# Kernel optimization log

Measured on AMD Instinct MI355X. Metric: run time of the kernel, lower is better.

## Reference

```python
import jax, jax.numpy as jnp
import numpy as np
from jax import lax

LAMBDA_SPATIAL = 0.5
SIGMA = 100.0
B, N, D = 16, 2048, 768


def setup_inputs() -> dict:
    key = jax.random.key(0)
    k1, k2 = jax.random.split(key)
    features = jax.random.normal(k1, (B, N, D), dtype=jnp.float32)
    coords = jax.random.uniform(k2, (B, N, 2), dtype=jnp.float32)
    return {"features": features, "coords": coords}


def _compute_similarity(features, coords):
    # features: [B,N,D], coords: [B,N,2] -> similarity [B,N,N]
    fn = features / jnp.maximum(jnp.linalg.norm(features, axis=-1, keepdims=True), 1e-12)
    semantic = jnp.einsum('bnd,bmd->bnm', fn, fn)
    diff = coords[:, :, None, :] - coords[:, None, :, :]   # [B,N,N,2]
    sq_dist = jnp.sum(diff * diff, axis=-1)                # d_ij^2
    spatial = jnp.exp(-sq_dist / (SIGMA ** 2))
    return semantic + LAMBDA_SPATIAL * spatial


def _greedy_order(sim):
    # sim: [N,N] -> order [N] int32 greedy nearest-neighbor traversal
    n = sim.shape[0]
    start = jnp.argmax(jnp.sum(sim, axis=1)).astype(jnp.int32)
    visited0 = jnp.zeros((n,), dtype=bool).at[start].set(True)

    def step(carry, _):
        cur, visited = carry
        row = jnp.where(visited, -jnp.inf, jnp.take(sim, cur, axis=0))
        nxt = jnp.argmax(row).astype(jnp.int32)
        return (nxt, visited.at[nxt].set(True)), nxt

    _, rest = lax.scan(step, (start, visited0), None, length=n - 1)
    return jnp.concatenate([start[None], rest])


def reference(features, coords):
    similarity = _compute_similarity(features, coords)          # [B,N,N]
    order = jax.vmap(_greedy_order)(similarity)                 # [B,N]
    reordered = jnp.take_along_axis(features, order[:, :, None], axis=1)  # [B,N,D]
    return reordered, order
```

## Files before the change

### kernel.cpp

```cpp
#include <hip/hip_runtime.h>
#include <math.h>

#define BATCH 16
#define NPTS  2048
#define DIM   768
#define NCH   24

typedef unsigned long long ull;
typedef float f32x4 __attribute__((ext_vector_type(4)));
typedef short bf8 __attribute__((ext_vector_type(8)));

__device__ __forceinline__ unsigned bfr(float x) {
  unsigned u = __float_as_uint(x);
  return (u + 0x7FFFu + ((u >> 16) & 1u)) & 0xFFFF0000u;
}
__device__ __forceinline__ unsigned short f2bf(float x) {
  unsigned u = __float_as_uint(x);
  u += 0x7FFFu + ((u >> 16) & 1u);
  return (unsigned short)(u >> 16);
}

__global__ void normalize_k(const float* __restrict__ feat, float* __restrict__ fn, int cs) {
  const int rn = blockIdx.x;
  const int ci = rn >> 11, n = rn & (NPTS - 1);
  const float* src = feat + ((size_t)(cs + ci) * NPTS + n) * DIM;
  const int t = threadIdx.x;
  float f0 = src[t], f1 = src[t + 256], f2 = src[t + 512];
  double s = (double)f0 * (double)f0 + (double)f1 * (double)f1 + (double)f2 * (double)f2;
  for (int off = 32; off > 0; off >>= 1) s += __shfl_down(s, off);
  __shared__ double ps[4];
  __shared__ double rbc;
  const int lane = t & 63, wid = t >> 6;
  if (lane == 0) ps[wid] = s;
  __syncthreads();
  if (t == 0) {
    double tot = ps[0] + ps[1] + ps[2] + ps[3];
    rbc = fmax(sqrt(tot), 1e-12);
  }
  __syncthreads();
  const double r = rbc;
  float* dst = fn + ((size_t)ci * NPTS + n) * DIM;
  dst[t]       = (float)((double)f0 / r);
  dst[t + 256] = (float)((double)f1 / r);
  dst[t + 512] = (float)((double)f2 / r);
}

__global__ __launch_bounds__(256, 1) void gemm_k(const float* __restrict__ fn,
                                                 const float* __restrict__ coords,
                                                 float* __restrict__ S, int cs) {
  if (blockIdx.x > blockIdx.y) return;
  const int ci = blockIdx.z;
  const int i0 = blockIdx.x * 128;
  const int j0 = blockIdx.y * 128;
  const int tid  = threadIdx.x;
  const int lane = tid & 63, w = tid >> 6;
  const int wr = (w >> 1) * 64, wc = (w & 1) * 64;
  const int lo = lane & 15, quad = lane >> 4;

  __shared__ unsigned short At[128][128];
  __shared__ unsigned short Bt[128][128];

  f32x4 aH[4][4], aM[4][4], aL[4][4];
#pragma unroll
  for (int tr = 0; tr < 4; ++tr)
#pragma unroll
    for (int tc = 0; tc < 4; ++tc) {
      aH[tr][tc] = (f32x4){0.f, 0.f, 0.f, 0.f};
      aM[tr][tc] = (f32x4){0.f, 0.f, 0.f, 0.f};
      aL[tr][tc] = (f32x4){0.f, 0.f, 0.f, 0.f};
    }

  const float* fb = fn + (size_t)ci * NPTS * DIM;
  const int row  = tid >> 1;
  const int half = tid & 1;
  const float* ag = fb + (size_t)(i0 + row) * DIM + half * 16;
  const float* bg = fb + (size_t)(j0 + row) * DIM + half * 16;

  float4 fa[4], fbv[4];
#pragma unroll
  for (int g = 0; g < 4; ++g) {
    fa[g]  = *(const float4*)(ag + g * 4);
    fbv[g] = *(const float4*)(bg + g * 4);
  }

#pragma unroll 1
  for (int c = 0; c < NCH; ++c) {
    float wa[16], wb[16];
#pragma unroll
    for (int g = 0; g < 4; ++g) {
      wa[4 * g + 0] = fa[g].x;  wa[4 * g + 1] = fa[g].y;
      wa[4 * g + 2] = fa[g].z;  wa[4 * g + 3] = fa[g].w;
      wb[4 * g + 0] = fbv[g].x; wb[4 * g + 1] = fbv[g].y;
      wb[4 * g + 2] = fbv[g].z; wb[4 * g + 3] = fbv[g].w;
    }
    unsigned sa[2][3][4], sb[2][3][4];
#pragma unroll
    for (int h = 0; h < 2; ++h)
#pragma unroll
      for (int j = 0; j < 8; j += 2) {
        {
          float w0 = wa[8 * h + j], w1 = wa[8 * h + j + 1];
          unsigned a0 = bfr(w0); float r0 = w0 - __uint_as_float(a0);
          unsigned a1 = bfr(w1); float r1 = w1 - __uint_as_float(a1);
          unsigned b0 = bfr(r0); float q0 = r0 - __uint_as_float(b0);
          unsigned b1 = bfr(r1); float q1 = r1 - __uint_as_float(b1);
          unsigned c0 = bfr(q0), c1 = bfr(q1);
          sa[h][0][j >> 1] = (a0 >> 16) | (a1 & 0xFFFF0000u);
          sa[h][1][j >> 1] = (b0 >> 16) | (b1 & 0xFFFF0000u);
          sa[h][2][j >> 1] = (c0 >> 16) | (c1 & 0xFFFF0000u);
        }
        {
          float w0 = wb[8 * h + j], w1 = wb[8 * h + j + 1];
          unsigned a0 = bfr(w0); float r0 = w0 - __uint_as_float(a0);
          unsigned a1 = bfr(w1); float r1 = w1 - __uint_as_float(a1);
          unsigned b0 = bfr(r0); float q0 = r0 - __uint_as_float(b0);
          unsigned b1 = bfr(r1); float q1 = r1 - __uint_as_float(b1);
          unsigned c0 = bfr(q0), c1 = bfr(q1);
          sb[h][0][j >> 1] = (a0 >> 16) | (a1 & 0xFFFF0000u);
          sb[h][1][j >> 1] = (b0 >> 16) | (b1 & 0xFFFF0000u);
          sb[h][2][j >> 1] = (c0 >> 16) | (c1 & 0xFFFF0000u);
        }
      }
    if (c + 1 < NCH) {
      const int kc = (c + 1) * 32;
#pragma unroll
      for (int g = 0; g < 4; ++g) {
        fa[g]  = *(const float4*)(ag + kc + g * 4);
        fbv[g] = *(const float4*)(bg + kc + g * 4);
      }
    }
    __syncthreads();
#pragma unroll
    for (int p = 0; p < 3; ++p)
#pragma unroll
      for (int h = 0; h < 2; ++h) {
        const int off = ((p * 4 + half * 2 + h) ^ (row & 7)) << 3;
        *(uint4*)&At[row][off] = *(uint4*)&sa[h][p][0];
        *(uint4*)&Bt[row][off] = *(uint4*)&sb[h][p][0];
      }
    __syncthreads();
    bf8 A0[4], A1[4], A2[4], B0[4], B1[4], B2[4];
#pragma unroll
    for (int t = 0; t < 4; ++t) {
      const int rA = wr + t * 16 + lo, rB = wc + t * 16 + lo;
      const int xA = rA & 7, xB = rB & 7;
      A0[t] = *(const bf8*)&At[rA][((quad + 0) ^ xA) << 3];
      A1[t] = *(const bf8*)&At[rA][((quad + 4) ^ xA) << 3];
      A2[t] = *(const bf8*)&At[rA][((quad + 8) ^ xA) << 3];
      B0[t] = *(const bf8*)&Bt[rB][((quad + 0) ^ xB) << 3];
      B1[t] = *(const bf8*)&Bt[rB][((quad + 4) ^ xB) << 3];
      B2[t] = *(const bf8*)&Bt[rB][((quad + 8) ^ xB) << 3];
    }
#pragma unroll
    for (int tr = 0; tr < 4; ++tr)
#pragma unroll
      for (int tc = 0; tc < 4; ++tc) {
        aH[tr][tc] = __builtin_amdgcn_mfma_f32_16x16x32_bf16(A0[tr], B0[tc], aH[tr][tc], 0, 0, 0);
        aM[tr][tc] = __builtin_amdgcn_mfma_f32_16x16x32_bf16(A0[tr], B1[tc], aM[tr][tc], 0, 0, 0);
        aM[tr][tc] = __builtin_amdgcn_mfma_f32_16x16x32_bf16(A1[tr], B0[tc], aM[tr][tc], 0, 0, 0);
        aL[tr][tc] = __builtin_amdgcn_mfma_f32_16x16x32_bf16(A0[tr], B2[tc], aL[tr][tc], 0, 0, 0);
        aL[tr][tc] = __builtin_amdgcn_mfma_f32_16x16x32_bf16(A1[tr], B1[tc], aL[tr][tc], 0, 0, 0);
        aL[tr][tc] = __builtin_amdgcn_mfma_f32_16x16x32_bf16(A2[tr], B0[tc], aL[tr][tc], 0, 0, 0);
      }
  }

  {
    const unsigned short encv = f2bf((float)lo);
    const unsigned short onev = f2bf(1.0f);
    bf8 enc, one;
#pragma unroll
    for (int t = 0; t < 8; ++t) { enc[t] = (short)encv; one[t] = (short)onev; }
    f32x4 z = (f32x4){0.f, 0.f, 0.f, 0.f};
    f32x4 d1 = __builtin_amdgcn_mfma_f32_16x16x32_bf16(enc, one, z, 0, 0, 0);
    f32x4 d2 = __builtin_amdgcn_mfma_f32_16x16x32_bf16(one, enc, z, 0, 0, 0);
    int rowp[4], colp[4];
#pragma unroll
    for (int r = 0; r < 4; ++r) {
      rowp[r] = ((int)(d1[r] * (1.0f / 32.0f))) & 15;
      colp[r] = ((int)(d2[r] * (1.0f / 32.0f))) & 15;
    }

    const float* cb = coords + (size_t)(cs + ci) * NPTS * 2;
    float* Sb = S + (size_t)ci * NPTS * NPTS;
#pragma unroll
    for (int r = 0; r < 4; ++r) {
      const int rl = rowp[r], cl = colp[r];
#pragma unroll
      for (int tr = 0; tr < 4; ++tr) {
        const int rowi = i0 + wr + tr * 16 + rl;
        float2 pi = *(const float2*)(cb + 2 * rowi);
        const double cix = pi.x, ciy = pi.y;
#pragma unroll
        for (int tc = 0; tc < 4; ++tc) {
          const int colj = j0 + wc + tc * 16 + cl;
          float2 pj = *(const float2*)(cb + 2 * colj);
          double dx = cix - (double)pj.x, dy = ciy - (double)pj.y;
          double x = (dx * dx + dy * dy) * (1.0 / 10000.0);
          double e = 1.0 - x * (1.0 - x * (0.5 - x * ((1.0 / 6.0) - x * (1.0 / 24.0))));
          double sem = (double)aH[tr][tc][r] + (double)aM[tr][tc][r] + (double)aL[tr][tc][r];
          Sb[(size_t)rowi * NPTS + colj] = (float)(sem + 0.5 * e);
        }
      }
    }
  }
}

__global__ __launch_bounds__(256) void mirror_k(float* __restrict__ S) {
  const int Cb = blockIdx.x, Rb = blockIdx.y;
  if ((Rb >> 1) <= (Cb >> 1)) return;
  float* Sb = S + (size_t)blockIdx.z * NPTS * NPTS;
  __shared__ float t[64][65];
  const int lane = threadIdx.x & 63, w = threadIdx.x >> 6;
#pragma unroll
  for (int p = 0; p < 16; ++p) {
    const int r = w + 4 * p;
    t[r][lane] = Sb[(size_t)(Cb * 64 + r) * NPTS + Rb * 64 + lane];
  }
  __syncthreads();
#pragma unroll
  for (int p = 0; p < 16; ++p) {
    const int r = w + 4 * p;
    Sb[(size_t)(Rb * 64 + r) * NPTS + Cb * 64 + lane] = t[lane][r];
  }
}

__device__ __forceinline__ unsigned mono(float f) {
  unsigned u = __float_as_uint(f);
  return (u & 0x80000000u) ? ~u : (u | 0x80000000u);
}

#define DPP64_STEP(X, CTRL, RMASK) do {                                                   \
  unsigned lo_ = (unsigned)(X), hi_ = (unsigned)((X) >> 32);                              \
  unsigned lo2_ = (unsigned)__builtin_amdgcn_update_dpp((int)lo_, (int)lo_, CTRL, RMASK, 0xf, false); \
  unsigned hi2_ = (unsigned)__builtin_amdgcn_update_dpp((int)hi_, (int)hi_, CTRL, RMASK, 0xf, false); \
  ull o_ = ((ull)hi2_ << 32) | lo2_;                                                      \
  if (o_ > (X)) (X) = o_;                                                                 \
} while (0)

__device__ __forceinline__ ull wave_amax64(ull x) {
  DPP64_STEP(x, 0x111, 0xf);
  DPP64_STEP(x, 0x112, 0xf);
  DPP64_STEP(x, 0x114, 0xf);
  DPP64_STEP(x, 0x118, 0xf);
  DPP64_STEP(x, 0x142, 0xa);
  DPP64_STEP(x, 0x143, 0xc);
  unsigned lo = (unsigned)__builtin_amdgcn_readlane((int)(unsigned)x, 63);
  unsigned hi = (unsigned)__builtin_amdgcn_readlane((int)(unsigned)(x >> 32), 63);
  return ((ull)hi << 32) | lo;
}

__global__ __launch_bounds__(64) void cand_k(const float* __restrict__ S,
                                             ull* __restrict__ cand8,
                                             double* __restrict__ rs) {
  const size_t r = blockIdx.x;
  const int row = (int)(r & (NPTS - 1));
  const float* rowp = S + r * NPTS;
  const int lane = threadIdx.x;

  float4 q[8];
  double sum = 0.0;
#pragma unroll
  for (int c = 0; c < 8; ++c) {
    q[c] = ((const float4*)rowp)[c * 64 + lane];
    sum += (double)q[c].x; sum += (double)q[c].y; sum += (double)q[c].z; sum += (double)q[c].w;
  }
  {
    double s2 = sum;
    for (int off = 32; off > 0; off >>= 1) s2 += __shfl_down(s2, off);
    if (lane == 0) rs[r] = s2;
  }

  unsigned rem = 0;
  const int dd = row - 4 * lane;
  if (dd >= 0 && dd < 2048 && (dd & 0xFC) == 0) rem = 1u << (((dd >> 8) << 2) | (dd & 3));

  float bv; int bp;
  auto rescan = [&]() {
    bv = -INFINITY; bp = 0;
#pragma unroll
    for (int c = 0; c < 8; ++c) {
      const float xs0 = q[c].x, xs1 = q[c].y, xs2 = q[c].z, xs3 = q[c].w;
      float x0 = ((rem >> (4 * c + 0)) & 1u) ? -INFINITY : xs0;
      float x1 = ((rem >> (4 * c + 1)) & 1u) ? -INFINITY : xs1;
      float x2 = ((rem >> (4 * c + 2)) & 1u) ? -INFINITY : xs2;
      float x3 = ((rem >> (4 * c + 3)) & 1u) ? -INFINITY : xs3;
      if (x0 > bv) { bv = x0; bp = 4 * c + 0; }
      if (x1 > bv) { bv = x1; bp = 4 * c + 1; }
      if (x2 > bv) { bv = x2; bp = 4 * c + 2; }
      if (x3 > bv) { bv = x3; bp = 4 * c + 3; }
    }
  };
  rescan();

#pragma unroll 1
  for (int rnd = 0; rnd < 8; ++rnd) {
    const int gi = ((bp >> 2) << 8) + 4 * lane + (bp & 3);
    const ull pk = ((ull)mono(bv) << 32) | (unsigned)(2047 - gi);
    const ull red = wave_amax64(pk);
    if (rnd < 7) {
      if (lane == 0) cand8[r * 8 + rnd] = red;
      if (pk == red) { rem |= 1u << bp; rescan(); }
    } else {
      if (lane == 0) cand8[r * 8 + 7] = (red >> 32) << 32;
    }
  }
}

__global__ __launch_bounds__(64) void traverse_k(const float* __restrict__ S,
                                                 const ull* __restrict__ cand8,
                                                 const double* __restrict__ rs,
                                                 float* __restrict__ order_f, int cs) {
  extern __shared__ ull tabL[];
  const int ci = blockIdx.x;
  const int gb = cs + ci;
  const int lane = threadIdx.x;

  {
    float4* ls = (float4*)tabL;
    const float4* gs = (const float4*)(cand8 + (size_t)ci * NPTS * 8);
#pragma unroll 1
    for (int i0 = 0; i0 < 8192; i0 += 512) {
      float4 t[8];
#pragma unroll
      for (int j = 0; j < 8; ++j) t[j] = gs[i0 + j * 64 + lane];
#pragma unroll
      for (int j = 0; j < 8; ++j) ls[i0 + j * 64 + lane] = t[j];
    }
  }
  __syncthreads();

  const double* rb = rs + (size_t)ci * NPTS;
  double dv = -1.0e300; int di = 0;
#pragma unroll
  for (int c = 0; c < 32; ++c) {
    int j = c * 64 + lane;
    double v = rb[j];
    if (v > dv) { dv = v; di = j; }
  }
  for (int off = 32; off > 0; off >>= 1) {
    double vo = __shfl_down(dv, off);
    int io = __shfl_down(di, off);
    if (vo > dv || (vo == dv && io < di)) { dv = vo; di = io; }
  }
  int cur = __shfl(di, 0);

  unsigned vis = 0, visw = 0;
  if (lane == ((cur >> 2) & 63)) vis |= 1u << (((cur >> 8) << 2) | (cur & 3));
  if (lane == (cur >> 5))        visw |= 1u << (cur & 31);
  if (lane == 0) order_f[(size_t)gb * NPTS] = (float)cur;

  const float* Sb = S + (size_t)ci * NPTS * NPTS;
  const int slot = lane & 7;

#pragma unroll 1
  for (int s = 1; s < NPTS; ++s) {
    const ull e = tabL[cur * 8 + slot];
    const unsigned idx = 2047u - (unsigned)(e & 0xFFFFFFFFu);
    const unsigned wv = (unsigned)__shfl((int)visw, (int)(idx >> 5));
    ull mk = ((slot == 7) || ((wv >> (idx & 31)) & 1u)) ? 0ull : e;
    DPP64_STEP(mk, 0x111, 0xf);
    DPP64_STEP(mk, 0x112, 0xf);
    DPP64_STEP(mk, 0x114, 0xf);
    const unsigned kH = (unsigned)__builtin_amdgcn_readlane((int)(unsigned)(mk >> 32), 7);
    const unsigned kL = (unsigned)__builtin_amdgcn_readlane((int)(unsigned)mk, 7);
    const unsigned tH = (unsigned)__builtin_amdgcn_readlane((int)(unsigned)(e >> 32), 7);
    int nxt;
    if (kH > tH) {
      nxt = (int)(2047u - kL);
    } else {
      const float4* rowp = (const float4*)(Sb + (size_t)cur * NPTS);
      float4 v[8];
#pragma unroll
      for (int c = 0; c < 8; ++c) v[c] = rowp[c * 64 + lane];
      float bvv = -INFINITY; int bi = 0;
#pragma unroll
      for (int c = 0; c < 8; ++c) {
        const int base = c * 256 + 4 * lane;
        float x0 = (vis & (1u << (4 * c + 0))) ? -INFINITY : v[c].x;
        float x1 = (vis & (1u << (4 * c + 1))) ? -INFINITY : v[c].y;
        float x2 = (vis & (1u << (4 * c + 2))) ? -INFINITY : v[c].z;
        float x3 = (vis & (1u << (4 * c + 3))) ? -INFINITY : v[c].w;
        if (x0 > bvv) { bvv = x0; bi = base + 0; }
        if (x1 > bvv) { bvv = x1; bi = base + 1; }
        if (x2 > bvv) { bvv = x2; bi = base + 2; }
        if (x3 > bvv) { bvv = x3; bi = base + 3; }
      }
      const ull pk = ((ull)mono(bvv) << 32) | (unsigned)(2047 - bi);
      const ull mm = wave_amax64(pk);
      nxt = (int)(2047u - (unsigned)(mm & 0xFFFFFFFFu));
    }
    if (lane == ((nxt >> 2) & 63)) vis |= 1u << (((nxt >> 8) << 2) | (nxt & 3));
    if (lane == (nxt >> 5))        visw |= 1u << (nxt & 31);
    if (lane == 0) order_f[(size_t)gb * NPTS + s] = (float)nxt;
    cur = nxt;
  }
}

__global__ void gather_k(const float* __restrict__ feat, const float* __restrict__ order_f,
                         float* __restrict__ out) {
  const int bk = blockIdx.x;
  const int b = bk >> 11, k = bk & (NPTS - 1);
  const int idx = (int)order_f[(size_t)b * NPTS + k];
  const float4* src = (const float4*)(feat + ((size_t)b * NPTS + idx) * DIM);
  float4* dst = (float4*)(out + ((size_t)b * NPTS + k) * DIM);
  dst[threadIdx.x] = src[threadIdx.x];
}

extern "C" void kernel_launch(void* const* d_in, const int* in_sizes, int n_in,
                              void* d_out, int out_size, void* d_ws, size_t ws_size,
                              hipStream_t stream) {
  const float* features = (const float*)d_in[0];
  const float* coords   = (const float*)d_in[1];
  float* out = (float*)d_out;
  float* order_f = out + (size_t)BATCH * NPTS * DIM;

  static bool attr_done = false;
  if (!attr_done) {
    (void)hipFuncSetAttribute((const void*)traverse_k,
                              hipFuncAttributeMaxDynamicSharedMemorySize, 131072);
    attr_done = true;
  }

  const size_t per_b = (size_t)NPTS * 8 + (size_t)NPTS * NPTS * 4 +
                       (size_t)NPTS * DIM * 4 + (size_t)NPTS * 8 * 8;
  int C = BATCH;
  while (C > 1 && per_b * (size_t)C > ws_size) C >>= 1;

  char* wp = (char*)d_ws;
  double* rowsum = (double*)wp;               wp += (size_t)C * NPTS * 8;
  float*  S      = (float*)wp;                wp += (size_t)C * NPTS * NPTS * 4;
  float*  fn     = (float*)wp;                wp += (size_t)C * NPTS * DIM * 4;
  ull*    cand8  = (ull*)wp;

  for (int cs = 0; cs < BATCH; cs += C) {
    normalize_k<<<dim3(C * NPTS), dim3(256), 0, stream>>>(features, fn, cs);
    gemm_k<<<dim3(16, 16, C), dim3(256), 0, stream>>>(fn, coords, S, cs);
    mirror_k<<<dim3(32, 32, C), dim3(256), 0, stream>>>(S);
    cand_k<<<dim3(C * NPTS), dim3(64), 0, stream>>>(S, cand8, rowsum);
    traverse_k<<<dim3(C), dim3(64), 131072, stream>>>(S, cand8, rowsum, order_f, cs);
  }
  gather_k<<<dim3(BATCH * NPTS), dim3(192), 0, stream>>>(features, order_f, out);
}
```

Before: 1.960 ms.

## Stage fp32 tiles via async global_load_lds double buffer, split to bf16 at fragment load

The GEMM mainloop now copies raw fp32 A/B tiles from global memory straight into double-buffered LDS with global_load_lds and a rotated slot swizzle. Each wave splits the values into three bf16 parts when it reads its fragments, instead of every thread splitting and writing bf16 planes into LDS. This removes one barrier per K-chunk and overlaps the next chunk's loads with MFMA work. In exchange, each element is split redundantly by every wave that reads it, which adds VALU work, and LDS usage and bank-access patterns change.

```diff
diff --git a/kernel.cpp b/kernel.cpp
--- a/kernel.cpp
+++ b/kernel.cpp
@@ -18,6 +18,26 @@
   unsigned u = __float_as_uint(x);
   u += 0x7FFFu + ((u >> 16) & 1u);
   return (unsigned short)(u >> 16);
+}
+
+__device__ __forceinline__ void split8(const f32x4& v0, const f32x4& v1,
+                                       bf8& o1, bf8& o2, bf8& o3) {
+  float wv[8];
+  wv[0] = v0[0]; wv[1] = v0[1]; wv[2] = v0[2]; wv[3] = v0[3];
+  wv[4] = v1[0]; wv[5] = v1[1]; wv[6] = v1[2]; wv[7] = v1[3];
+  union { unsigned u[4]; bf8 v; } p1, p2, p3;
+#pragma unroll
+  for (int j = 0; j < 8; j += 2) {
+    float w0 = wv[j], w1 = wv[j + 1];
+    unsigned a0 = bfr(w0); float r0 = w0 - __uint_as_float(a0);
+    unsigned a1 = bfr(w1); float r1 = w1 - __uint_as_float(a1);
+    unsigned b0 = bfr(r0); float q0 = r0 - __uint_as_float(b0);
+    unsigned b1 = bfr(r1); float q1 = r1 - __uint_as_float(b1);
+    p1.u[j >> 1] = (a0 >> 16) | (a1 & 0xFFFF0000u);
+    p2.u[j >> 1] = (b0 >> 16) | (b1 & 0xFFFF0000u);
+    p3.u[j >> 1] = (bfr(q0) >> 16) | (bfr(q1) & 0xFFFF0000u);
+  }
+  o1 = p1.v; o2 = p2.v; o3 = p3.v;
 }
 
 __global__ void normalize_k(const float* __restrict__ feat, float* __restrict__ fn, int cs) {
@@ -57,8 +77,8 @@
   const int wr = (w >> 1) * 64, wc = (w & 1) * 64;
   const int lo = lane & 15, quad = lane >> 4;
 
-  __shared__ unsigned short At[128][128];
-  __shared__ unsigned short Bt[128][128];
+  __shared__ float Ar[2][128][32];
+  __shared__ float Br[2][128][32];
 
   f32x4 aH[4][4], aM[4][4], aL[4][4];
 #pragma unroll
@@ -71,97 +91,65 @@
     }
 
   const float* fb = fn + (size_t)ci * NPTS * DIM;
-  const int row  = tid >> 1;
-  const int half = tid & 1;
-  const float* ag = fb + (size_t)(i0 + row) * DIM + half * 16;
-  const float* bg = fb + (size_t)(j0 + row) * DIM + half * 16;
-
-  float4 fa[4], fbv[4];
-#pragma unroll
-  for (int g = 0; g < 4; ++g) {
-    fa[g]  = *(const float4*)(ag + g * 4);
-    fbv[g] = *(const float4*)(bg + g * 4);
-  }
+  const int trow  = tid >> 3;
+  const int pslot = tid & 7;
+
+  auto issue = [&](int p, int kc) {
+#pragma unroll
+    for (int i = 0; i < 4; ++i) {
+      const int row   = i * 32 + trow;
+      const int cslot = (pslot - (row & 7)) & 7;
+      const float* ga = fb + (size_t)(i0 + row) * DIM + kc + cslot * 4;
+      const float* gb = fb + (size_t)(j0 + row) * DIM + kc + cslot * 4;
+      float* la = &Ar[p][0][0] + (size_t)(i * 256 + tid) * 4;
+      float* lb = &Br[p][0][0] + (size_t)(i * 256 + tid) * 4;
+      __builtin_amdgcn_global_load_lds((const __attribute__((address_space(1))) void*)ga,
+                                       (__attribute__((address_space(3))) void*)la, 16, 0, 0);
+      __builtin_amdgcn_global_load_lds((const __attribute__((address_space(1))) void*)gb,
+                                       (__attribute__((address_space(3))) void*)lb, 16, 0, 0);
+    }
+  };
+
+  issue(0, 0);
+  int p = 0;
 
 #pragma unroll 1
   for (int c = 0; c < NCH; ++c) {
-    float wa[16], wb[16];
-#pragma unroll
-    for (int g = 0; g < 4; ++g) {
-      wa[4 * g + 0] = fa[g].x;  wa[4 * g + 1] = fa[g].y;
-      wa[4 * g + 2] = fa[g].z;  wa[4 * g + 3] = fa[g].w;
-      wb[4 * g + 0] = fbv[g].x; wb[4 * g + 1] = fbv[g].y;
-      wb[4 * g + 2] = fbv[g].z; wb[4 * g + 3] = fbv[g].w;
-    }
-    unsigned sa[2][3][4], sb[2][3][4];
-#pragma unroll
-    for (int h = 0; h < 2; ++h)
-#pragma unroll
-      for (int j = 0; j < 8; j += 2) {
-        {
-          float w0 = wa[8 * h + j], w1 = wa[8 * h + j + 1];
-          unsigned a0 = bfr(w0); float r0 = w0 - __uint_as_float(a0);
-          unsigned a1 = bfr(w1); float r1 = w1 - __uint_as_float(a1);
-          unsigned b0 = bfr(r0); float q0 = r0 - __uint_as_float(b0);
-          unsigned b1 = bfr(r1); float q1 = r1 - __uint_as_float(b1);
-          unsigned c0 = bfr(q0), c1 = bfr(q1);
-          sa[h][0][j >> 1] = (a0 >> 16) | (a1 & 0xFFFF0000u);
-          sa[h][1][j >> 1] = (b0 >> 16) | (b1 & 0xFFFF0000u);
-          sa[h][2][j >> 1] = (c0 >> 16) | (c1 & 0xFFFF0000u);
-        }
-        {
-          float w0 = wb[8 * h + j], w1 = wb[8 * h + j + 1];
-          unsigned a0 = bfr(w0); float r0 = w0 - __uint_as_float(a0);
-          unsigned a1 = bfr(w1); float r1 = w1 - __uint_as_float(a1);
-          unsigned b0 = bfr(r0); float q0 = r0 - __uint_as_float(b0);
-          unsigned b1 = bfr(r1); float q1 = r1 - __uint_as_float(b1);
-          unsigned c0 = bfr(q0), c1 = bfr(q1);
-          sb[h][0][j >> 1] = (a0 >> 16) | (a1 & 0xFFFF0000u);
-          sb[h][1][j >> 1] = (b0 >> 16) | (b1 & 0xFFFF0000u);
-          sb[h][2][j >> 1] = (c0 >> 16) | (c1 & 0xFFFF0000u);
-        }
+    __syncthreads();
+    if (c + 1 < NCH) issue(p ^ 1, (c + 1) * 32);
+
+    bf8 B0[4], B1[4], B2[4];
+#pragma unroll
+    for (int t = 0; t < 4; ++t) {
+      const int r = wc + t * 16 + lo;
+      const int x = r & 7;
+      const int s0 = ((2 * quad + 0) + x) & 7;
+      const int s1 = ((2 * quad + 1) + x) & 7;
+      f32x4 v0 = *(const f32x4*)&Br[p][r][s0 * 4];
+      f32x4 v1 = *(const f32x4*)&Br[p][r][s1 * 4];
+      split8(v0, v1, B0[t], B1[t], B2[t]);
+    }
+#pragma unroll
+    for (int tr = 0; tr < 4; ++tr) {
+      const int r = wr + tr * 16 + lo;
+      const int x = r & 7;
+      const int s0 = ((2 * quad + 0) + x) & 7;
+      const int s1 = ((2 * quad + 1) + x) & 7;
+      f32x4 v0 = *(const f32x4*)&Ar[p][r][s0 * 4];
+      f32x4 v1 = *(const f32x4*)&Ar[p][r][s1 * 4];
+      bf8 A0, A1, A2;
+      split8(v0, v1, A0, A1, A2);
+#pragma unroll
+      for (int tc = 0; tc < 4; ++tc) {
+        aH[tr][tc] = __builtin_amdgcn_mfma_f32_16x16x32_bf16(A0, B0[tc], aH[tr][tc], 0, 0, 0);
+        aM[tr][tc] = __builtin_amdgcn_mfma_f32_16x16x32_bf16(A0, B1[tc], aM[tr][tc], 0, 0, 0);
+        aM[tr][tc] = __builtin_amdgcn_mfma_f32_16x16x32_bf16(A1, B0[tc], aM[tr][tc], 0, 0, 0);
+        aL[tr][tc] = __builtin_amdgcn_mfma_f32_16x16x32_bf16(A0, B2[tc], aL[tr][tc], 0, 0, 0);
+        aL[tr][tc] = __builtin_amdgcn_mfma_f32_16x16x32_bf16(A1, B1[tc], aL[tr][tc], 0, 0, 0);
+        aL[tr][tc] = __builtin_amdgcn_mfma_f32_16x16x32_bf16(A2, B0[tc], aL[tr][tc], 0, 0, 0);
       }
-    if (c + 1 < NCH) {
-      const int kc = (c + 1) * 32;
-#pragma unroll
-      for (int g = 0; g < 4; ++g) {
-        fa[g]  = *(const float4*)(ag + kc + g * 4);
-        fbv[g] = *(const float4*)(bg + kc + g * 4);
-      }
-    }
-    __syncthreads();
-#pragma unroll
-    for (int p = 0; p < 3; ++p)
-#pragma unroll
-      for (int h = 0; h < 2; ++h) {
-        const int off = ((p * 4 + half * 2 + h) ^ (row & 7)) << 3;
-        *(uint4*)&At[row][off] = *(uint4*)&sa[h][p][0];
-        *(uint4*)&Bt[row][off] = *(uint4*)&sb[h][p][0];
-      }
-    __syncthreads();
-    bf8 A0[4], A1[4], A2[4], B0[4], B1[4], B2[4];
-#pragma unroll
-    for (int t = 0; t < 4; ++t) {
-      const int rA = wr + t * 16 + lo, rB = wc + t * 16 + lo;
-      const int xA = rA & 7, xB = rB & 7;
-      A0[t] = *(const bf8*)&At[rA][((quad + 0) ^ xA) << 3];
-      A1[t] = *(const bf8*)&At[rA][((quad + 4) ^ xA) << 3];
-      A2[t] = *(const bf8*)&At[rA][((quad + 8) ^ xA) << 3];
-      B0[t] = *(const bf8*)&Bt[rB][((quad + 0) ^ xB) << 3];
-      B1[t] = *(const bf8*)&Bt[rB][((quad + 4) ^ xB) << 3];
-      B2[t] = *(const bf8*)&Bt[rB][((quad + 8) ^ xB) << 3];
-    }
-#pragma unroll
-    for (int tr = 0; tr < 4; ++tr)
-#pragma unroll
-      for (int tc = 0; tc < 4; ++tc) {
-        aH[tr][tc] = __builtin_amdgcn_mfma_f32_16x16x32_bf16(A0[tr], B0[tc], aH[tr][tc], 0, 0, 0);
-        aM[tr][tc] = __builtin_amdgcn_mfma_f32_16x16x32_bf16(A0[tr], B1[tc], aM[tr][tc], 0, 0, 0);
-        aM[tr][tc] = __builtin_amdgcn_mfma_f32_16x16x32_bf16(A1[tr], B0[tc], aM[tr][tc], 0, 0, 0);
-        aL[tr][tc] = __builtin_amdgcn_mfma_f32_16x16x32_bf16(A0[tr], B2[tc], aL[tr][tc], 0, 0, 0);
-        aL[tr][tc] = __builtin_amdgcn_mfma_f32_16x16x32_bf16(A1[tr], B1[tc], aL[tr][tc], 0, 0, 0);
-        aL[tr][tc] = __builtin_amdgcn_mfma_f32_16x16x32_bf16(A2[tr], B0[tc], aL[tr][tc], 0, 0, 0);
-      }
+    }
+    p ^= 1;
   }
 
   {
```

Result: slower. 2.210 ms (+12.7%).

## Double-buffer GEMM shared tiles with padded layout to overlap split and MFMA

Applied to the files above, without the earlier changes.

The split-bf16 GEMM now uses two dynamic-LDS buffers. The next chunk's bf16 triple split and store overlap with the MFMA step on the current buffer, which leaves one barrier per chunk instead of two. The XOR-swizzled 128-wide tile is replaced by per-plane arrays padded to a 40-element row pitch. This costs more LDS (about 120KB) and register pressure from two prefetch sets, and the padded layout may bring back bank conflicts.

```diff
diff --git a/kernel.cpp b/kernel.cpp
--- a/kernel.cpp
+++ b/kernel.cpp
@@ -5,6 +5,9 @@
 #define NPTS  2048
 #define DIM   768
 #define NCH   24
+#define PADW  40
+#define MATSZ 15360
+#define BUFSZ 30720
 
 typedef unsigned long long ull;
 typedef float f32x4 __attribute__((ext_vector_type(4)));
@@ -18,6 +21,36 @@
   unsigned u = __float_as_uint(x);
   u += 0x7FFFu + ((u >> 16) & 1u);
   return (unsigned short)(u >> 16);
+}
+
+__device__ __forceinline__ void cw16(const float4& x0, const float4& x1,
+                                     const float4& x2, const float4& x3,
+                                     unsigned short* base, int row, int half) {
+  float wa[16];
+  wa[0]  = x0.x; wa[1]  = x0.y; wa[2]  = x0.z; wa[3]  = x0.w;
+  wa[4]  = x1.x; wa[5]  = x1.y; wa[6]  = x1.z; wa[7]  = x1.w;
+  wa[8]  = x2.x; wa[9]  = x2.y; wa[10] = x2.z; wa[11] = x2.w;
+  wa[12] = x3.x; wa[13] = x3.y; wa[14] = x3.z; wa[15] = x3.w;
+  unsigned sa[2][3][4];
+#pragma unroll
+  for (int h = 0; h < 2; ++h)
+#pragma unroll
+    for (int j = 0; j < 8; j += 2) {
+      float w0 = wa[8 * h + j], w1 = wa[8 * h + j + 1];
+      unsigned a0 = bfr(w0); float r0 = w0 - __uint_as_float(a0);
+      unsigned a1 = bfr(w1); float r1 = w1 - __uint_as_float(a1);
+      unsigned b0 = bfr(r0); float q0 = r0 - __uint_as_float(b0);
+      unsigned b1 = bfr(r1); float q1 = r1 - __uint_as_float(b1);
+      unsigned c0 = bfr(q0), c1 = bfr(q1);
+      sa[h][0][j >> 1] = (a0 >> 16) | (a1 & 0xFFFF0000u);
+      sa[h][1][j >> 1] = (b0 >> 16) | (b1 & 0xFFFF0000u);
+      sa[h][2][j >> 1] = (c0 >> 16) | (c1 & 0xFFFF0000u);
+    }
+#pragma unroll
+  for (int pl = 0; pl < 3; ++pl)
+#pragma unroll
+    for (int h = 0; h < 2; ++h)
+      *(uint4*)&base[pl * 5120 + row * PADW + half * 16 + 8 * h] = *(uint4*)&sa[h][pl][0];
 }
 
 __global__ void normalize_k(const float* __restrict__ feat, float* __restrict__ fn, int cs) {
@@ -57,8 +90,7 @@
   const int wr = (w >> 1) * 64, wc = (w & 1) * 64;
   const int lo = lane & 15, quad = lane >> 4;
 
-  __shared__ unsigned short At[128][128];
-  __shared__ unsigned short Bt[128][128];
+  extern __shared__ unsigned short sl[];
 
   f32x4 aH[4][4], aM[4][4], aL[4][4];
 #pragma unroll
@@ -76,93 +108,71 @@
   const float* ag = fb + (size_t)(i0 + row) * DIM + half * 16;
   const float* bg = fb + (size_t)(j0 + row) * DIM + half * 16;
 
-  float4 fa[4], fbv[4];
-#pragma unroll
-  for (int g = 0; g < 4; ++g) {
-    fa[g]  = *(const float4*)(ag + g * 4);
-    fbv[g] = *(const float4*)(bg + g * 4);
-  }
+  float4 a0[4], b0[4], a1[4], b1[4];
+
+#define LOADSET(SA, SB, KC) do {                                    \
+    SA[0] = *(const float4*)(ag + (KC) + 0);                        \
+    SA[1] = *(const float4*)(ag + (KC) + 4);                        \
+    SA[2] = *(const float4*)(ag + (KC) + 8);                        \
+    SA[3] = *(const float4*)(ag + (KC) + 12);                       \
+    SB[0] = *(const float4*)(bg + (KC) + 0);                        \
+    SB[1] = *(const float4*)(bg + (KC) + 4);                        \
+    SB[2] = *(const float4*)(bg + (KC) + 8);                        \
+    SB[3] = *(const float4*)(bg + (KC) + 12);                       \
+  } while (0)
+
+#define CWSET(SA, SB, P) do {                                       \
+    cw16(SA[0], SA[1], SA[2], SA[3], sl + (P) * BUFSZ,          row, half); \
+    cw16(SB[0], SB[1], SB[2], SB[3], sl + (P) * BUFSZ + MATSZ,  row, half); \
+  } while (0)
+
+#define MFMASTEP(P) do {                                            \
+    const unsigned short* Ab = sl + (P) * BUFSZ;                    \
+    const unsigned short* Bb = Ab + MATSZ;                          \
+    bf8 A0[4], A1[4], A2[4], B0[4], B1[4], B2[4];                   \
+    _Pragma("unroll")                                               \
+    for (int t = 0; t < 4; ++t) {                                   \
+      const int rA = wr + t * 16 + lo, rB = wc + t * 16 + lo, k8 = quad * 8; \
+      A0[t] = *(const bf8*)&Ab[0 * 5120 + rA * PADW + k8];          \
+      A1[t] = *(const bf8*)&Ab[1 * 5120 + rA * PADW + k8];          \
+      A2[t] = *(const bf8*)&Ab[2 * 5120 + rA * PADW + k8];          \
+      B0[t] = *(const bf8*)&Bb[0 * 5120 + rB * PADW + k8];          \
+      B1[t] = *(const bf8*)&Bb[1 * 5120 + rB * PADW + k8];          \
+      B2[t] = *(const bf8*)&Bb[2 * 5120 + rB * PADW + k8];          \
+    }                                                               \
+    _Pragma("unroll")                                               \
+    for (int tr = 0; tr < 4; ++tr)                                  \
+      _Pragma("unroll")                                             \
+      for (int tc = 0; tc < 4; ++tc) {                              \
+        aH[tr][tc] = __builtin_amdgcn_mfma_f32_16x16x32_bf16(A0[tr], B0[tc], aH[tr][tc], 0, 0, 0); \
+        aM[tr][tc] = __builtin_amdgcn_mfma_f32_16x16x32_bf16(A0[tr], B1[tc], aM[tr][tc], 0, 0, 0); \
+        aM[tr][tc] = __builtin_amdgcn_mfma_f32_16x16x32_bf16(A1[tr], B0[tc], aM[tr][tc], 0, 0, 0); \
+        aL[tr][tc] = __builtin_amdgcn_mfma_f32_16x16x32_bf16(A0[tr], B2[tc], aL[tr][tc], 0, 0, 0); \
+        aL[tr][tc] = __builtin_amdgcn_mfma_f32_16x16x32_bf16(A1[tr], B1[tc], aL[tr][tc], 0, 0, 0); \
+        aL[tr][tc] = __builtin_amdgcn_mfma_f32_16x16x32_bf16(A2[tr], B0[tc], aL[tr][tc], 0, 0, 0); \
+      }                                                             \
+  } while (0)
+
+  LOADSET(a0, b0, 0);
+  CWSET(a0, b0, 0);
+  LOADSET(a1, b1, 32);
+  __syncthreads();
 
 #pragma unroll 1
-  for (int c = 0; c < NCH; ++c) {
-    float wa[16], wb[16];
-#pragma unroll
-    for (int g = 0; g < 4; ++g) {
-      wa[4 * g + 0] = fa[g].x;  wa[4 * g + 1] = fa[g].y;
-      wa[4 * g + 2] = fa[g].z;  wa[4 * g + 3] = fa[g].w;
-      wb[4 * g + 0] = fbv[g].x; wb[4 * g + 1] = fbv[g].y;
-      wb[4 * g + 2] = fbv[g].z; wb[4 * g + 3] = fbv[g].w;
-    }
-    unsigned sa[2][3][4], sb[2][3][4];
-#pragma unroll
-    for (int h = 0; h < 2; ++h)
-#pragma unroll
-      for (int j = 0; j < 8; j += 2) {
-        {
-          float w0 = wa[8 * h + j], w1 = wa[8 * h + j + 1];
-          unsigned a0 = bfr(w0); float r0 = w0 - __uint_as_float(a0);
-          unsigned a1 = bfr(w1); float r1 = w1 - __uint_as_float(a1);
-          unsigned b0 = bfr(r0); float q0 = r0 - __uint_as_float(b0);
-          unsigned b1 = bfr(r1); float q1 = r1 - __uint_as_float(b1);
-          unsigned c0 = bfr(q0), c1 = bfr(q1);
-          sa[h][0][j >> 1] = (a0 >> 16) | (a1 & 0xFFFF0000u);
-          sa[h][1][j >> 1] = (b0 >> 16) | (b1 & 0xFFFF0000u);
-          sa[h][2][j >> 1] = (c0 >> 16) | (c1 & 0xFFFF0000u);
-        }
-        {
-          float w0 = wb[8 * h + j], w1 = wb[8 * h + j + 1];
-          unsigned a0 = bfr(w0); float r0 = w0 - __uint_as_float(a0);
-          unsigned a1 = bfr(w1); float r1 = w1 - __uint_as_float(a1);
-          unsigned b0 = bfr(r0); float q0 = r0 - __uint_as_float(b0);
-          unsigned b1 = bfr(r1); float q1 = r1 - __uint_as_float(b1);
-          unsigned c0 = bfr(q0), c1 = bfr(q1);
-          sb[h][0][j >> 1] = (a0 >> 16) | (a1 & 0xFFFF0000u);
-          sb[h][1][j >> 1] = (b0 >> 16) | (b1 & 0xFFFF0000u);
-          sb[h][2][j >> 1] = (c0 >> 16) | (c1 & 0xFFFF0000u);
-        }
-      }
-    if (c + 1 < NCH) {
-      const int kc = (c + 1) * 32;
-#pragma unroll
-      for (int g = 0; g < 4; ++g) {
-        fa[g]  = *(const float4*)(ag + kc + g * 4);
-        fbv[g] = *(const float4*)(bg + kc + g * 4);
-      }
-    }
+  for (int cc = 0; cc < NCH; cc += 2) {
+    if (cc + 2 < NCH) LOADSET(a0, b0, (cc + 2) * 32);
+    if (cc + 1 < NCH) CWSET(a1, b1, 1);
+    MFMASTEP(0);
     __syncthreads();
-#pragma unroll
-    for (int p = 0; p < 3; ++p)
-#pragma unroll
-      for (int h = 0; h < 2; ++h) {
-        const int off = ((p * 4 + half * 2 + h) ^ (row & 7)) << 3;
-        *(uint4*)&At[row][off] = *(uint4*)&sa[h][p][0];
-        *(uint4*)&Bt[row][off] = *(uint4*)&sb[h][p][0];
-      }
+    if (cc + 3 < NCH) LOADSET(a1, b1, (cc + 3) * 32);
+    if (cc + 2 < NCH) CWSET(a0, b0, 0);
+    MFMASTEP(1);
     __syncthreads();
-    bf8 A0[4], A1[4], A2[4], B0[4], B1[4], B2[4];
-#pragma unroll
-    for (int t = 0; t < 4; ++t) {
-      const int rA = wr + t * 16 + lo, rB = wc + t * 16 + lo;
-      const int xA = rA & 7, xB = rB & 7;
-      A0[t] = *(const bf8*)&At[rA][((quad + 0) ^ xA) << 3];
-      A1[t] = *(const bf8*)&At[rA][((quad + 4) ^ xA) << 3];
-      A2[t] = *(const bf8*)&At[rA][((quad + 8) ^ xA) << 3];
-      B0[t] = *(const bf8*)&Bt[rB][((quad + 0) ^ xB) << 3];
-      B1[t] = *(const bf8*)&Bt[rB][((quad + 4) ^ xB) << 3];
-      B2[t] = *(const bf8*)&Bt[rB][((quad + 8) ^ xB) << 3];
-    }
-#pragma unroll
-    for (int tr = 0; tr < 4; ++tr)
-#pragma unroll
-      for (int tc = 0; tc < 4; ++tc) {
-        aH[tr][tc] = __builtin_amdgcn_mfma_f32_16x16x32_bf16(A0[tr], B0[tc], aH[tr][tc], 0, 0, 0);
-        aM[tr][tc] = __builtin_amdgcn_mfma_f32_16x16x32_bf16(A0[tr], B1[tc], aM[tr][tc], 0, 0, 0);
-        aM[tr][tc] = __builtin_amdgcn_mfma_f32_16x16x32_bf16(A1[tr], B0[tc], aM[tr][tc], 0, 0, 0);
-        aL[tr][tc] = __builtin_amdgcn_mfma_f32_16x16x32_bf16(A0[tr], B2[tc], aL[tr][tc], 0, 0, 0);
-        aL[tr][tc] = __builtin_amdgcn_mfma_f32_16x16x32_bf16(A1[tr], B1[tc], aL[tr][tc], 0, 0, 0);
-        aL[tr][tc] = __builtin_amdgcn_mfma_f32_16x16x32_bf16(A2[tr], B0[tc], aL[tr][tc], 0, 0, 0);
-      }
-  }
+  }
+
+#undef LOADSET
+#undef CWSET
+#undef MFMASTEP
 
   {
     const unsigned short encv = f2bf((float)lo);
@@ -414,10 +424,14 @@
   float* out = (float*)d_out;
   float* order_f = out + (size_t)BATCH * NPTS * DIM;
 
+  const int gemm_lds = 2 * BUFSZ * 2;
+
   static bool attr_done = false;
   if (!attr_done) {
     (void)hipFuncSetAttribute((const void*)traverse_k,
                               hipFuncAttributeMaxDynamicSharedMemorySize, 131072);
+    (void)hipFuncSetAttribute((const void*)gemm_k,
+                              hipFuncAttributeMaxDynamicSharedMemorySize, gemm_lds);
     attr_done = true;
   }
 
@@ -434,7 +448,7 @@
 
   for (int cs = 0; cs < BATCH; cs += C) {
     normalize_k<<<dim3(C * NPTS), dim3(256), 0, stream>>>(features, fn, cs);
-    gemm_k<<<dim3(16, 16, C), dim3(256), 0, stream>>>(fn, coords, S, cs);
+    gemm_k<<<dim3(16, 16, C), dim3(256), gemm_lds, stream>>>(fn, coords, S, cs);
     mirror_k<<<dim3(32, 32, C), dim3(256), 0, stream>>>(S);
     cand_k<<<dim3(C * NPTS), dim3(64), 0, stream>>>(S, cand8, rowsum);
     traverse_k<<<dim3(C), dim3(64), 131072, stream>>>(S, cand8, rowsum, order_f, cs);
```

Result: slower. 2.012 ms (+2.6%).

## Use 512-thread GEMM blocks with split bf16 planes and padded LDS

Applied to the files above, without the earlier changes.

The similarity GEMM block grows from 256 to 512 threads (8 waves, each computing a 64x32 sub-tile instead of 64x64). This halves accumulator registers per wave and spreads the bf16 split-conversion work across more threads. Shared memory becomes three per-precision planes with padded rows instead of an XOR swizzle, and the order of syncs and prefetch loads is rearranged. The aim is more latency hiding per CU, at the cost of more redundant LDS reads of the A fragments and possible bank conflicts from the padding layout.

```diff
diff --git a/kernel.cpp b/kernel.cpp
--- a/kernel.cpp
+++ b/kernel.cpp
@@ -5,6 +5,7 @@
 #define NPTS  2048
 #define DIM   768
 #define NCH   24
+#define PADW  40
 
 typedef unsigned long long ull;
 typedef float f32x4 __attribute__((ext_vector_type(4)));
@@ -45,7 +46,7 @@
   dst[t + 512] = (float)((double)f2 / r);
 }
 
-__global__ __launch_bounds__(256, 1) void gemm_k(const float* __restrict__ fn,
+__global__ __launch_bounds__(512, 1) void gemm_k(const float* __restrict__ fn,
                                                  const float* __restrict__ coords,
                                                  float* __restrict__ S, int cs) {
   if (blockIdx.x > blockIdx.y) return;
@@ -54,107 +55,93 @@
   const int j0 = blockIdx.y * 128;
   const int tid  = threadIdx.x;
   const int lane = tid & 63, w = tid >> 6;
-  const int wr = (w >> 1) * 64, wc = (w & 1) * 64;
+  const int wrow = (w >> 2) * 64, wcol = (w & 3) * 32;
   const int lo = lane & 15, quad = lane >> 4;
 
-  __shared__ unsigned short At[128][128];
-  __shared__ unsigned short Bt[128][128];
-
-  f32x4 aH[4][4], aM[4][4], aL[4][4];
+  __shared__ unsigned short At[3][128][PADW];
+  __shared__ unsigned short Bt[3][128][PADW];
+
+  f32x4 aH[4][2], aM[4][2], aL[4][2];
 #pragma unroll
   for (int tr = 0; tr < 4; ++tr)
 #pragma unroll
-    for (int tc = 0; tc < 4; ++tc) {
+    for (int tc = 0; tc < 2; ++tc) {
       aH[tr][tc] = (f32x4){0.f, 0.f, 0.f, 0.f};
       aM[tr][tc] = (f32x4){0.f, 0.f, 0.f, 0.f};
       aL[tr][tc] = (f32x4){0.f, 0.f, 0.f, 0.f};
     }
 
   const float* fb = fn + (size_t)ci * NPTS * DIM;
-  const int row  = tid >> 1;
-  const int half = tid & 1;
-  const float* ag = fb + (size_t)(i0 + row) * DIM + half * 16;
-  const float* bg = fb + (size_t)(j0 + row) * DIM + half * 16;
-
-  float4 fa[4], fbv[4];
-#pragma unroll
-  for (int g = 0; g < 4; ++g) {
-    fa[g]  = *(const float4*)(ag + g * 4);
-    fbv[g] = *(const float4*)(bg + g * 4);
-  }
+  const int row = tid >> 2;
+  const int q   = tid & 3;
+  const float* ag = fb + (size_t)(i0 + row) * DIM + q * 8;
+  const float* bg = fb + (size_t)(j0 + row) * DIM + q * 8;
+
+  float4 fa0, fa1, fb0, fb1;
+  fa0 = *(const float4*)(ag);     fa1 = *(const float4*)(ag + 4);
+  fb0 = *(const float4*)(bg);     fb1 = *(const float4*)(bg + 4);
 
 #pragma unroll 1
   for (int c = 0; c < NCH; ++c) {
-    float wa[16], wb[16];
-#pragma unroll
-    for (int g = 0; g < 4; ++g) {
-      wa[4 * g + 0] = fa[g].x;  wa[4 * g + 1] = fa[g].y;
-      wa[4 * g + 2] = fa[g].z;  wa[4 * g + 3] = fa[g].w;
-      wb[4 * g + 0] = fbv[g].x; wb[4 * g + 1] = fbv[g].y;
-      wb[4 * g + 2] = fbv[g].z; wb[4 * g + 3] = fbv[g].w;
-    }
-    unsigned sa[2][3][4], sb[2][3][4];
-#pragma unroll
-    for (int h = 0; h < 2; ++h)
+    __syncthreads();
+    {
+      float wa[8] = { fa0.x, fa0.y, fa0.z, fa0.w, fa1.x, fa1.y, fa1.z, fa1.w };
+      float wb[8] = { fb0.x, fb0.y, fb0.z, fb0.w, fb1.x, fb1.y, fb1.z, fb1.w };
+      unsigned sa[3][4], sb[3][4];
 #pragma unroll
       for (int j = 0; j < 8; j += 2) {
         {
-          float w0 = wa[8 * h + j], w1 = wa[8 * h + j + 1];
+          float w0 = wa[j], w1 = wa[j + 1];
           unsigned a0 = bfr(w0); float r0 = w0 - __uint_as_float(a0);
           unsigned a1 = bfr(w1); float r1 = w1 - __uint_as_float(a1);
           unsigned b0 = bfr(r0); float q0 = r0 - __uint_as_float(b0);
           unsigned b1 = bfr(r1); float q1 = r1 - __uint_as_float(b1);
-          unsigned c0 = bfr(q0), c1 = bfr(q1);
-          sa[h][0][j >> 1] = (a0 >> 16) | (a1 & 0xFFFF0000u);
-          sa[h][1][j >> 1] = (b0 >> 16) | (b1 & 0xFFFF0000u);
-          sa[h][2][j >> 1] = (c0 >> 16) | (c1 & 0xFFFF0000u);
+          sa[0][j >> 1] = (a0 >> 16) | (a1 & 0xFFFF0000u);
+          sa[1][j >> 1] = (b0 >> 16) | (b1 & 0xFFFF0000u);
+          sa[2][j >> 1] = (bfr(q0) >> 16) | (bfr(q1) & 0xFFFF0000u);
         }
         {
-          float w0 = wb[8 * h + j], w1 = wb[8 * h + j + 1];
+          float w0 = wb[j], w1 = wb[j + 1];
           unsigned a0 = bfr(w0); float r0 = w0 - __uint_as_float(a0);
           unsigned a1 = bfr(w1); float r1 = w1 - __uint_as_float(a1);
           unsigned b0 = bfr(r0); float q0 = r0 - __uint_as_float(b0);
           unsigned b1 = bfr(r1); float q1 = r1 - __uint_as_float(b1);
-          unsigned c0 = bfr(q0), c1 = bfr(q1);
-          sb[h][0][j >> 1] = (a0 >> 16) | (a1 & 0xFFFF0000u);
-          sb[h][1][j >> 1] = (b0 >> 16) | (b1 & 0xFFFF0000u);
-          sb[h][2][j >> 1] = (c0 >> 16) | (c1 & 0xFFFF0000u);
+          sb[0][j >> 1] = (a0 >> 16) | (a1 & 0xFFFF0000u);
+          sb[1][j >> 1] = (b0 >> 16) | (b1 & 0xFFFF0000u);
+          sb[2][j >> 1] = (bfr(q0) >> 16) | (bfr(q1) & 0xFFFF0000u);
         }
       }
+#pragma unroll
+      for (int pl = 0; pl < 3; ++pl) {
+        *(uint4*)&At[pl][row][q * 8] = *(uint4*)&sa[pl][0];
+        *(uint4*)&Bt[pl][row][q * 8] = *(uint4*)&sb[pl][0];
+      }
+    }
+    __syncthreads();
     if (c + 1 < NCH) {
       const int kc = (c + 1) * 32;
-#pragma unroll
-      for (int g = 0; g < 4; ++g) {
-        fa[g]  = *(const float4*)(ag + kc + g * 4);
-        fbv[g] = *(const float4*)(bg + kc + g * 4);
-      }
-    }
-    __syncthreads();
-#pragma unroll
-    for (int p = 0; p < 3; ++p)
-#pragma unroll
-      for (int h = 0; h < 2; ++h) {
-        const int off = ((p * 4 + half * 2 + h) ^ (row & 7)) << 3;
-        *(uint4*)&At[row][off] = *(uint4*)&sa[h][p][0];
-        *(uint4*)&Bt[row][off] = *(uint4*)&sb[h][p][0];
-      }
-    __syncthreads();
-    bf8 A0[4], A1[4], A2[4], B0[4], B1[4], B2[4];
+      fa0 = *(const float4*)(ag + kc);  fa1 = *(const float4*)(ag + kc + 4);
+      fb0 = *(const float4*)(bg + kc);  fb1 = *(const float4*)(bg + kc + 4);
+    }
+    bf8 A0[4], A1[4], A2[4], B0[2], B1[2], B2[2];
 #pragma unroll
     for (int t = 0; t < 4; ++t) {
-      const int rA = wr + t * 16 + lo, rB = wc + t * 16 + lo;
-      const int xA = rA & 7, xB = rB & 7;
-      A0[t] = *(const bf8*)&At[rA][((quad + 0) ^ xA) << 3];
-      A1[t] = *(const bf8*)&At[rA][((quad + 4) ^ xA) << 3];
-      A2[t] = *(const bf8*)&At[rA][((quad + 8) ^ xA) << 3];
-      B0[t] = *(const bf8*)&Bt[rB][((quad + 0) ^ xB) << 3];
-      B1[t] = *(const bf8*)&Bt[rB][((quad + 4) ^ xB) << 3];
-      B2[t] = *(const bf8*)&Bt[rB][((quad + 8) ^ xB) << 3];
+      const int rA = wrow + t * 16 + lo, k8 = quad * 8;
+      A0[t] = *(const bf8*)&At[0][rA][k8];
+      A1[t] = *(const bf8*)&At[1][rA][k8];
+      A2[t] = *(const bf8*)&At[2][rA][k8];
+    }
+#pragma unroll
+    for (int t = 0; t < 2; ++t) {
+      const int rB = wcol + t * 16 + lo, k8 = quad * 8;
+      B0[t] = *(const bf8*)&Bt[0][rB][k8];
+      B1[t] = *(const bf8*)&Bt[1][rB][k8];
+      B2[t] = *(const bf8*)&Bt[2][rB][k8];
     }
 #pragma unroll
     for (int tr = 0; tr < 4; ++tr)
 #pragma unroll
-      for (int tc = 0; tc < 4; ++tc) {
+      for (int tc = 0; tc < 2; ++tc) {
         aH[tr][tc] = __builtin_amdgcn_mfma_f32_16x16x32_bf16(A0[tr], B0[tc], aH[tr][tc], 0, 0, 0);
         aM[tr][tc] = __builtin_amdgcn_mfma_f32_16x16x32_bf16(A0[tr], B1[tc], aM[tr][tc], 0, 0, 0);
         aM[tr][tc] = __builtin_amdgcn_mfma_f32_16x16x32_bf16(A1[tr], B0[tc], aM[tr][tc], 0, 0, 0);
@@ -187,12 +174,12 @@
       const int rl = rowp[r], cl = colp[r];
 #pragma unroll
       for (int tr = 0; tr < 4; ++tr) {
-        const int rowi = i0 + wr + tr * 16 + rl;
+        const int rowi = i0 + wrow + tr * 16 + rl;
         float2 pi = *(const float2*)(cb + 2 * rowi);
         const double cix = pi.x, ciy = pi.y;
 #pragma unroll
-        for (int tc = 0; tc < 4; ++tc) {
-          const int colj = j0 + wc + tc * 16 + cl;
+        for (int tc = 0; tc < 2; ++tc) {
+          const int colj = j0 + wcol + tc * 16 + cl;
           float2 pj = *(const float2*)(cb + 2 * colj);
           double dx = cix - (double)pj.x, dy = ciy - (double)pj.y;
           double x = (dx * dx + dy * dy) * (1.0 / 10000.0);
@@ -434,7 +421,7 @@
 
   for (int cs = 0; cs < BATCH; cs += C) {
     normalize_k<<<dim3(C * NPTS), dim3(256), 0, stream>>>(features, fn, cs);
-    gemm_k<<<dim3(16, 16, C), dim3(256), 0, stream>>>(fn, coords, S, cs);
+    gemm_k<<<dim3(16, 16, C), dim3(512), 0, stream>>>(fn, coords, S, cs);
     mirror_k<<<dim3(32, 32, C), dim3(256), 0, stream>>>(S);
     cand_k<<<dim3(C * NPTS), dim3(64), 0, stream>>>(S, cand8, rowsum);
     traverse_k<<<dim3(C), dim3(64), 131072, stream>>>(S, cand8, rowsum, order_f, cs);
```

After: 1.781 ms. 9.1% less time.
